# Kernel tuning notes

Hardware: AMD Instinct MI355X
Metric: run time of the kernel (lower is better)

Reference implementation:

```python
import jax, jax.numpy as jnp
import numpy as np

N_NODES = 100000
N_EDGES = 3200000
D_IN = 64
D_OUT = 64


def setup_inputs() -> dict:
    key = jax.random.key(0)
    k0, k1, k2, k3 = jax.random.split(key, 4)
    x = jax.random.normal(k0, (N_NODES, D_IN), dtype=jnp.float32)
    edge_index = jax.random.randint(k1, (2, N_EDGES), 0, N_NODES, dtype=jnp.int64)
    edge_weight = jax.random.uniform(k2, (N_EDGES,), dtype=jnp.float32)
    W = jax.random.normal(k3, (D_IN, D_OUT), dtype=jnp.float32) / jnp.sqrt(jnp.float32(D_IN))
    b = jnp.zeros((D_OUT,), dtype=jnp.float32)
    return {"x": x, "edge_index": edge_index, "edge_weight": edge_weight, "W": W, "b": b}


def reference(x, edge_index, edge_weight, W, b):
    # GiGCNConv forward: asymmetric (random-walk, D^-1 A) gcn_norm with self loops,
    # then GCNConv(normalize=False): linear -> edge-weighted scatter-add -> bias.
    N = x.shape[0]
    src, dst = edge_index[0], edge_index[1]

    # add self loops (fill value 1.0 since improved=False)
    loop = jnp.arange(N, dtype=src.dtype)
    src = jnp.concatenate([src, loop])
    dst = jnp.concatenate([dst, loop])
    ew = jnp.concatenate([edge_weight.astype(x.dtype), jnp.ones((N,), dtype=x.dtype)])

    # asymmetric normalization: in-degree (at dst) inverse scaling
    deg = jax.ops.segment_sum(ew, dst, num_segments=N)          # [N]
    deg_inv = jnp.where(deg > 0, 1.0 / deg, 0.0)                # inf -> 0
    norm = deg_inv[dst] * ew                                    # [E+N]

    # GCNConv: project then aggregate messages at destination nodes
    h = x @ W                                                   # [N, D_OUT]
    msg = norm[:, None] * h[src]                                # [E+N, D_OUT] gather
    out = jax.ops.segment_sum(msg, dst, num_segments=N)         # scatter-add
    return out + b
```

## Files before the change

### kernel.cpp

```cpp
#include <hip/hip_runtime.h>


#define D 64
#define BSH 9
#define NPB 512
#define MAXB1 256
#define BATCHA 4096
#define C1S 32
#define WSCALE 8192.0f
#define WINV (1.0f / 8192.0f)

static __device__ __forceinline__ unsigned short f2bf(float f) {
    unsigned u = __float_as_uint(f);
    u += 0x7FFFu + ((u >> 16) & 1u);
    return (unsigned short)(u >> 16);
}
static __device__ __forceinline__ float bf2f(unsigned short s) {
    return __uint_as_float(((unsigned)s) << 16);
}
static __device__ __forceinline__ float bflo(unsigned u) {
    return __uint_as_float(u << 16);
}
static __device__ __forceinline__ float bfhi(unsigned u) {
    return __uint_as_float(u & 0xFFFF0000u);
}


__global__ __launch_bounds__(256) void hist_kernel(const int* __restrict__ dst,
                                                   int* __restrict__ hist, int E, int B1) {
    __shared__ int lh[MAXB1];
    int tid = threadIdx.x;
    if (tid < MAXB1) lh[tid] = 0;
    __syncthreads();
    int t = blockIdx.x * 256 + tid;
    int stride = gridDim.x * 256;
    if ((E & 3) == 0 && (((size_t)dst & 15) == 0)) {
        const int4* d4 = (const int4*)dst;
        int n4 = E >> 2;
        for (int e = t; e < n4; e += stride) {
            int4 v = d4[e];
            atomicAdd(&lh[v.x >> BSH], 1);
            atomicAdd(&lh[v.y >> BSH], 1);
            atomicAdd(&lh[v.z >> BSH], 1);
            atomicAdd(&lh[v.w >> BSH], 1);
        }
    } else {
        for (int e = t; e < E; e += stride) {
            int d = __builtin_nontemporal_load(dst + e);
            atomicAdd(&lh[d >> BSH], 1);
        }
    }
    __syncthreads();
    if (tid < B1) {
        int v = lh[tid];
        if (v) atomicAdd(&hist[tid], v);
    }
}


__global__ __launch_bounds__(256) void scan_kernel(const int* __restrict__ hist,
                                                   int* __restrict__ off1,
                                                   int* __restrict__ cur1, int B1, int E) {
    __shared__ int s[256];
    int tid = threadIdx.x;
    int v = (tid < B1) ? hist[tid] : 0;
    s[tid] = v;
    __syncthreads();
    for (int o = 1; o < 256; o <<= 1) {
        int t = (tid >= o) ? s[tid - o] : 0;
        __syncthreads();
        s[tid] += t;
        __syncthreads();
    }
    if (tid < B1) {
        int ex = s[tid] - v;
        off1[tid] = ex;
        cur1[tid * C1S] = ex;
    }
    if (tid == 0) off1[B1] = E;
}


__global__ __launch_bounds__(256) void partA_kernel(const int* __restrict__ src,
                                                    const int* __restrict__ dst,
                                                    const float* __restrict__ ew,
                                                    int* __restrict__ cur1,
                                                    int2* __restrict__ pairs1,
                                                    int E, int nb, int aligned) {
    __shared__ int bcnt[MAXB1];
    __shared__ int bbase[MAXB1];
    __shared__ int brank[MAXB1];
    int tid = threadIdx.x;
    for (int ib = blockIdx.x; ib < nb; ib += gridDim.x) {
        int base = ib * BATCHA;
        int blen = E - base;
        if (blen > BATCHA) blen = BATCHA;
        if (tid < MAXB1) { bcnt[tid] = 0; brank[tid] = 0; }
        __syncthreads();
        int dv[16], sv[16];
        float wv[16];
        int off = tid * 16;
        if (aligned && off + 16 <= blen) {
#pragma unroll
            for (int kk = 0; kk < 4; ++kk) {
                int4 d4 = ((const int4*)(dst + base + off))[kk];
                int4 s4 = ((const int4*)(src + base + off))[kk];
                float4 w4 = ((const float4*)(ew + base + off))[kk];
                dv[kk * 4 + 0] = d4.x; dv[kk * 4 + 1] = d4.y;
                dv[kk * 4 + 2] = d4.z; dv[kk * 4 + 3] = d4.w;
                sv[kk * 4 + 0] = s4.x; sv[kk * 4 + 1] = s4.y;
                sv[kk * 4 + 2] = s4.z; sv[kk * 4 + 3] = s4.w;
                wv[kk * 4 + 0] = w4.x; wv[kk * 4 + 1] = w4.y;
                wv[kk * 4 + 2] = w4.z; wv[kk * 4 + 3] = w4.w;
            }
#pragma unroll
            for (int m = 0; m < 16; ++m) atomicAdd(&bcnt[dv[m] >> BSH], 1);
        } else {
#pragma unroll
            for (int m = 0; m < 16; ++m) {
                bool v = (off + m) < blen;
                int e = base + off + m;
                dv[m] = v ? __builtin_nontemporal_load(dst + e) : -1;
                sv[m] = v ? __builtin_nontemporal_load(src + e) : 0;
                wv[m] = v ? __builtin_nontemporal_load(ew + e) : 0.0f;
                if (v) atomicAdd(&bcnt[dv[m] >> BSH], 1);
            }
        }
        __syncthreads();
        if (tid < MAXB1 && bcnt[tid] > 0)
            bbase[tid] = atomicAdd(&cur1[tid * C1S], bcnt[tid]);
        __syncthreads();
#pragma unroll
        for (int m = 0; m < 16; ++m) {
            if (dv[m] >= 0) {
                int bin = dv[m] >> BSH;
                int r = atomicAdd(&brank[bin], 1);
                pairs1[bbase[bin] + r] =
                    make_int2(sv[m] | ((dv[m] & (NPB - 1)) << 17),
                              __float_as_int(wv[m]));
            }
        }
        __syncthreads();
    }
}


__global__ __launch_bounds__(512) void sortmerge_kernel(const int2* __restrict__ pairs1,
                                                        const int* __restrict__ off1,
                                                        unsigned* __restrict__ cw,
                                                        int* __restrict__ node_off,
                                                        int N, int B1) {
    __shared__ int lh[NPB];
    __shared__ int s[NPB];
    __shared__ int cur[NPB];
    int tid = threadIdx.x;
    int c = blockIdx.x;
    int e0 = off1[c], e1 = off1[c + 1];

    lh[tid] = 0;
    __syncthreads();

    for (int ib = e0; ib < e1; ib += 512 * 8) {
        long long pv[8];
#pragma unroll
        for (int m = 0; m < 8; ++m) {
            int i = ib + m * 512 + tid;
            pv[m] = (i < e1)
                ? __builtin_nontemporal_load((const long long*)(pairs1 + i))
                : -1LL;
        }
#pragma unroll
        for (int m = 0; m < 8; ++m) {
            int i = ib + m * 512 + tid;
            if (i < e1) atomicAdd(&lh[((int)pv[m] >> 17) & (NPB - 1)], 1);
        }
    }
    __syncthreads();

    s[tid] = lh[tid];
    __syncthreads();
    for (int o = 1; o < NPB; o <<= 1) {
        int t = (tid >= o) ? s[tid - o] : 0;
        __syncthreads();
        s[tid] += t;
        __syncthreads();
    }
    int ex = s[tid] - lh[tid];
    int gbase = c << BSH;
    if (gbase + tid <= N) node_off[gbase + tid] = e0 + ex;
    if (c == B1 - 1 && tid == 0) node_off[N] = e1;
    cur[tid] = ex;
    __syncthreads();

    for (int ib = e0; ib < e1; ib += 512 * 8) {
        long long pv[8];
#pragma unroll
        for (int m = 0; m < 8; ++m) {
            int i = ib + m * 512 + tid;
            pv[m] = (i < e1)
                ? __builtin_nontemporal_load((const long long*)(pairs1 + i))
                : -1LL;
        }
#pragma unroll
        for (int m = 0; m < 8; ++m) {
            int i = ib + m * 512 + tid;
            if (i < e1) {
                int px = (int)pv[m];
                float w = __int_as_float((int)(pv[m] >> 32));
                int node = (px >> 17) & (NPB - 1);
                int pos = atomicAdd(&cur[node], 1);
                int wq = (int)fminf(fmaxf(w, 0.0f) * WSCALE + 0.5f, 32767.0f);
                cw[e0 + pos] = (unsigned)(px & 0x1FFFF) | ((unsigned)wq << 17);
            }
        }
    }
}


__global__ __launch_bounds__(256) void gemmW_kernel(const float* __restrict__ x,
                                                    const float* __restrict__ W,
                                                    unsigned short* __restrict__ hbf, int N) {
    __shared__ float Ws[D * D];
    __shared__ float xs[32][D];
    int tid = threadIdx.x;
    int j = tid & 63;
    int g = tid >> 6;
    int base = blockIdx.x * 32;
    for (int i = tid; i < D * D; i += 256) Ws[i] = W[i];
    for (int rr = g; rr < 32; rr += 4) {
        int r = base + rr;
        if (r < N) xs[rr][j] = x[(size_t)r * D + j];
    }
    __syncthreads();
    float wc[D];
#pragma unroll
    for (int k = 0; k < D; ++k) wc[k] = Ws[k * D + j];
    for (int rr = g; rr < 32; rr += 4) {
        int r = base + rr;
        if (r < N) {
            float s0 = 0.0f, s1 = 0.0f, s2 = 0.0f, s3 = 0.0f;
#pragma unroll
            for (int k = 0; k < D; k += 4) {
                s0 = fmaf(xs[rr][k + 0], wc[k + 0], s0);
                s1 = fmaf(xs[rr][k + 1], wc[k + 1], s1);
                s2 = fmaf(xs[rr][k + 2], wc[k + 2], s2);
                s3 = fmaf(xs[rr][k + 3], wc[k + 3], s3);
            }
            hbf[(size_t)r * D + j] = f2bf((s0 + s1) + (s2 + s3));
        }
    }
}


__global__ __launch_bounds__(256) void accum_kernel(const unsigned* __restrict__ cw,
                                                    const int* __restrict__ node_off,
                                                    const unsigned short* __restrict__ hbf,
                                                    const float* __restrict__ bias,
                                                    float* __restrict__ out, int N) {
    int t = blockIdx.x * 256 + threadIdx.x;
    int n = t >> 6;
    int l = t & 63;
    if (n >= N) return;
    int eg = l >> 4;
    int cl = l & 15;
    int base = node_off[n];
    int cnt = node_off[n + 1] - base;
    const unsigned* pp = cw + base;
    const unsigned short* hcol = hbf + cl * 4;

    float a0 = 0.0f, a1 = 0.0f, a2 = 0.0f, a3 = 0.0f;
    float degs = 0.0f;
    int i = eg;
    for (; i + 12 < cnt; i += 16) {
        unsigned va = pp[i];
        unsigned vb = pp[i + 4];
        unsigned vc = pp[i + 8];
        unsigned vd = pp[i + 12];
        uint2 ha = *(const uint2*)(hcol + (size_t)(va & 0x1FFFF) * D);
        uint2 hb = *(const uint2*)(hcol + (size_t)(vb & 0x1FFFF) * D);
        uint2 hc = *(const uint2*)(hcol + (size_t)(vc & 0x1FFFF) * D);
        uint2 hd = *(const uint2*)(hcol + (size_t)(vd & 0x1FFFF) * D);
        float wa = (float)(va >> 17) * WINV;
        float wb = (float)(vb >> 17) * WINV;
        float wc = (float)(vc >> 17) * WINV;
        float wd = (float)(vd >> 17) * WINV;
        degs += (wa + wb) + (wc + wd);
        a0 = fmaf(wa, bflo(ha.x), a0);
        a1 = fmaf(wa, bfhi(ha.x), a1);
        a2 = fmaf(wa, bflo(ha.y), a2);
        a3 = fmaf(wa, bfhi(ha.y), a3);
        a0 = fmaf(wb, bflo(hb.x), a0);
        a1 = fmaf(wb, bfhi(hb.x), a1);
        a2 = fmaf(wb, bflo(hb.y), a2);
        a3 = fmaf(wb, bfhi(hb.y), a3);
        a0 = fmaf(wc, bflo(hc.x), a0);
        a1 = fmaf(wc, bfhi(hc.x), a1);
        a2 = fmaf(wc, bflo(hc.y), a2);
        a3 = fmaf(wc, bfhi(hc.y), a3);
        a0 = fmaf(wd, bflo(hd.x), a0);
        a1 = fmaf(wd, bfhi(hd.x), a1);
        a2 = fmaf(wd, bflo(hd.y), a2);
        a3 = fmaf(wd, bfhi(hd.y), a3);
    }
    for (; i < cnt; i += 4) {
        unsigned v = pp[i];
        uint2 hv = *(const uint2*)(hcol + (size_t)(v & 0x1FFFF) * D);
        float w = (float)(v >> 17) * WINV;
        degs += w;
        a0 = fmaf(w, bflo(hv.x), a0);
        a1 = fmaf(w, bfhi(hv.x), a1);
        a2 = fmaf(w, bflo(hv.y), a2);
        a3 = fmaf(w, bfhi(hv.y), a3);
    }

    a0 += __shfl_xor(a0, 16); a0 += __shfl_xor(a0, 32);
    a1 += __shfl_xor(a1, 16); a1 += __shfl_xor(a1, 32);
    a2 += __shfl_xor(a2, 16); a2 += __shfl_xor(a2, 32);
    a3 += __shfl_xor(a3, 16); a3 += __shfl_xor(a3, 32);
    degs += __shfl_xor(degs, 16); degs += __shfl_xor(degs, 32);

    if (eg == 0) {
        uint2 hs = *(const uint2*)(hcol + (size_t)n * D);
        a0 += bflo(hs.x);
        a1 += bfhi(hs.x);
        a2 += bflo(hs.y);
        a3 += bfhi(hs.y);
        degs += 1.0f;
        float di = 1.0f / degs;
        const float4 bv = *(const float4*)(bias + cl * 4);
        float4 o;
        o.x = fmaf(di, a0, bv.x);
        o.y = fmaf(di, a1, bv.y);
        o.z = fmaf(di, a2, bv.z);
        o.w = fmaf(di, a3, bv.w);
        __builtin_nontemporal_store(o.x, out + (size_t)n * D + cl * 4 + 0);
        __builtin_nontemporal_store(o.y, out + (size_t)n * D + cl * 4 + 1);
        __builtin_nontemporal_store(o.z, out + (size_t)n * D + cl * 4 + 2);
        __builtin_nontemporal_store(o.w, out + (size_t)n * D + cl * 4 + 3);
    }
}


__global__ __launch_bounds__(256) void deg_kernel(const int* __restrict__ dst,
                                                  const float* __restrict__ ew,
                                                  float* __restrict__ deg, int E) {
    int t = blockIdx.x * 256 + threadIdx.x;
    int stride = gridDim.x * 256;
    for (int e = t; e < E; e += stride) atomicAdd(&deg[dst[e]], ew[e]);
}

__global__ __launch_bounds__(256) void deginv_kernel(float* __restrict__ deg, int N) {
    int t = blockIdx.x * 256 + threadIdx.x;
    int stride = gridDim.x * 256;
    for (int n = t; n < N; n += stride) {
        float tot = deg[n] + 1.0f;
        deg[n] = (tot > 0.0f) ? (1.0f / tot) : 0.0f;
    }
}

__global__ __launch_bounds__(256) void gemm16f_kernel(const float* __restrict__ x,
                                                      const float* __restrict__ W,
                                                      float* __restrict__ h, int N) {
    __shared__ float Ws[D * D];
    __shared__ float xs[16][D];
    int tid = threadIdx.x;
    int j = tid & 63;
    int q = tid >> 6;
    int base = blockIdx.x * 16;
    for (int i = tid; i < D * D; i += 256) Ws[i] = W[i];
    for (int rr = q; rr < 16; rr += 4) {
        int r = base + rr;
        if (r < N) xs[rr][j] = x[(size_t)r * D + j];
    }
    __syncthreads();
    for (int rr = q; rr < 16; rr += 4) {
        int r = base + rr;
        if (r < N) {
            float sum = 0.0f;
#pragma unroll
            for (int k = 0; k < D; ++k) sum = fmaf(xs[rr][k], Ws[k * D + j], sum);
            h[(size_t)r * D + j] = sum;
        }
    }
}

__global__ __launch_bounds__(256) void init_kernel(const float* __restrict__ h,
                                                   const float* __restrict__ deginv,
                                                   const float* __restrict__ b,
                                                   float* __restrict__ out, int N) {
    int t = blockIdx.x * 256 + threadIdx.x;
    int stride = gridDim.x * 256;
    int nq = N * (D / 4);
    const float4* h4 = (const float4*)h;
    const float4* b4 = (const float4*)b;
    float4* o4 = (float4*)out;
    for (int q = t; q < nq; q += stride) {
        int n = q >> 4;
        int c4 = q & 15;
        float4 hv = h4[q];
        float4 bv = b4[c4];
        float di = deginv[n];
        float4 o;
        o.x = bv.x + di * hv.x;
        o.y = bv.y + di * hv.y;
        o.z = bv.z + di * hv.z;
        o.w = bv.w + di * hv.w;
        o4[q] = o;
    }
}

__global__ __launch_bounds__(256) void scatter_kernel(const int* __restrict__ src,
                                                      const int* __restrict__ dst,
                                                      const float* __restrict__ ew,
                                                      const float* __restrict__ deginv,
                                                      const float* __restrict__ h,
                                                      float* __restrict__ out, int E) {
    int t = blockIdx.x * 256 + threadIdx.x;
    int wave = t >> 6;
    int lane = t & 63;
    int nwaves = (gridDim.x * 256) >> 6;
    for (int e = wave; e < E; e += nwaves) {
        int s = src[e];
        int d = dst[e];
        float norm = deginv[d] * ew[e];
        atomicAdd(&out[d * D + lane], norm * h[s * D + lane]);
    }
}


extern "C" void kernel_launch(void* const* d_in, const int* in_sizes, int n_in,
                              void* d_out, int out_size, void* d_ws, size_t ws_size,
                              hipStream_t stream) {
    const float* x  = (const float*)d_in[0];
    const int*   ei = (const int*)d_in[1];
    const float* ew = (const float*)d_in[2];
    const float* W  = (const float*)d_in[3];
    const float* b  = (const float*)d_in[4];
    float* out = (float*)d_out;

    int N = in_sizes[0] / D;
    int E = in_sizes[2];
    const int* srcp = ei;
    const int* dstp = ei + E;

    int B1 = (N + NPB - 1) >> BSH;

    size_t ints_n = 256 + 320 + (size_t)MAXB1 * C1S + ((size_t)N + 64);
    size_t p1_off  = ((ints_n * 4) + 255) & ~(size_t)255;
    size_t hbf_off = (p1_off + (size_t)E * 8 + 255) & ~(size_t)255;
    size_t cw_off  = (hbf_off + (size_t)N * D * 2 + 255) & ~(size_t)255;
    size_t need = cw_off + (size_t)E * 4;

    if (N <= 131072 && ws_size >= need) {
        int* hist     = (int*)d_ws;
        int* off1     = hist + 256;
        int* cur1     = off1 + 320;
        int* node_off = cur1 + (size_t)MAXB1 * C1S;
        int2* pairs1  = (int2*)((char*)d_ws + p1_off);
        unsigned short* hbf = (unsigned short*)((char*)d_ws + hbf_off);
        unsigned* cw  = (unsigned*)((char*)d_ws + cw_off);

        int aligned = (((E & 3) == 0) && (((size_t)dstp & 15) == 0)) ? 1 : 0;

        hipMemsetAsync(hist, 0, 256 * 4, stream);
        hist_kernel<<<1024, 256, 0, stream>>>(dstp, hist, E, B1);
        scan_kernel<<<1, 256, 0, stream>>>(hist, off1, cur1, B1, E);
        int nb = (E + BATCHA - 1) / BATCHA;
        int gA = nb < 2048 ? nb : 2048;
        partA_kernel<<<gA, 256, 0, stream>>>(srcp, dstp, ew, cur1, pairs1, E, nb, aligned);
        sortmerge_kernel<<<B1, 512, 0, stream>>>(pairs1, off1, cw, node_off, N, B1);
        gemmW_kernel<<<(N + 31) / 32, 256, 0, stream>>>(x, W, hbf, N);
        accum_kernel<<<(N + 3) / 4, 256, 0, stream>>>(cw, node_off, hbf, b, out, N);
    } else {
        size_t Npad = ((size_t)N + 63) & ~(size_t)63;
        float* deg = (float*)d_ws;
        float* h = deg + Npad;
        hipMemsetAsync(deg, 0, (size_t)N * sizeof(float), stream);
        deg_kernel<<<2048, 256, 0, stream>>>(dstp, ew, deg, E);
        deginv_kernel<<<(N + 255) / 256, 256, 0, stream>>>(deg, N);
        gemm16f_kernel<<<(N + 15) / 16, 256, 0, stream>>>(x, W, h, N);
        init_kernel<<<2048, 256, 0, stream>>>(h, deg, b, out, N);
        scatter_kernel<<<2048, 256, 0, stream>>>(srcp, dstp, ew, deg, h, out, E);
    }
}
```

Baseline: 192.6 us.

## Split bucketed edge pairs into packed cw words plus 16-bit local dst

partA now packs source index and quantized weight into a 32-bit word and writes the node-local destination as a separate 16-bit array, replacing the 8-byte int2 pairs. sortmerge reads only the 2-byte array for its histogram pass and moves the packed word directly in the scatter pass, with no requantization. The aim is to cut intermediate memory traffic between the partition and sort stages. Partition batches also double to 32 edges per thread and the histogram grid is halved, which raises register pressure and lowers parallelism per launch.

```diff
diff --git a/kernel.cpp b/kernel.cpp
--- a/kernel.cpp
+++ b/kernel.cpp
@@ -5,7 +5,7 @@
 #define BSH 9
 #define NPB 512
 #define MAXB1 256
-#define BATCHA 4096
+#define BATCHA 8192
 #define C1S 32
 #define WSCALE 8192.0f
 #define WINV (1.0f / 8192.0f)
@@ -15,14 +15,15 @@
     u += 0x7FFFu + ((u >> 16) & 1u);
     return (unsigned short)(u >> 16);
 }
-static __device__ __forceinline__ float bf2f(unsigned short s) {
-    return __uint_as_float(((unsigned)s) << 16);
-}
 static __device__ __forceinline__ float bflo(unsigned u) {
     return __uint_as_float(u << 16);
 }
 static __device__ __forceinline__ float bfhi(unsigned u) {
     return __uint_as_float(u & 0xFFFF0000u);
+}
+static __device__ __forceinline__ unsigned packcw(int s, float w) {
+    int wq = (int)fminf(fmaxf(w, 0.0f) * WSCALE + 0.5f, 32767.0f);
+    return (unsigned)s | ((unsigned)wq << 17);
 }
 
 
@@ -85,7 +86,8 @@
                                                     const int* __restrict__ dst,
                                                     const float* __restrict__ ew,
                                                     int* __restrict__ cur1,
-                                                    int2* __restrict__ pairs1,
+                                                    unsigned* __restrict__ cw0,
+                                                    unsigned short* __restrict__ dls,
                                                     int E, int nb, int aligned) {
     __shared__ int bcnt[MAXB1];
     __shared__ int bbase[MAXB1];
@@ -97,33 +99,41 @@
         if (blen > BATCHA) blen = BATCHA;
         if (tid < MAXB1) { bcnt[tid] = 0; brank[tid] = 0; }
         __syncthreads();
-        int dv[16], sv[16];
-        float wv[16];
-        int off = tid * 16;
-        if (aligned && off + 16 <= blen) {
-#pragma unroll
-            for (int kk = 0; kk < 4; ++kk) {
+        unsigned cwq[32];
+        int meta[32];
+        int off = tid * 32;
+        if (aligned && off + 32 <= blen) {
+#pragma unroll
+            for (int kk = 0; kk < 8; ++kk) {
                 int4 d4 = ((const int4*)(dst + base + off))[kk];
                 int4 s4 = ((const int4*)(src + base + off))[kk];
                 float4 w4 = ((const float4*)(ew + base + off))[kk];
-                dv[kk * 4 + 0] = d4.x; dv[kk * 4 + 1] = d4.y;
-                dv[kk * 4 + 2] = d4.z; dv[kk * 4 + 3] = d4.w;
-                sv[kk * 4 + 0] = s4.x; sv[kk * 4 + 1] = s4.y;
-                sv[kk * 4 + 2] = s4.z; sv[kk * 4 + 3] = s4.w;
-                wv[kk * 4 + 0] = w4.x; wv[kk * 4 + 1] = w4.y;
-                wv[kk * 4 + 2] = w4.z; wv[kk * 4 + 3] = w4.w;
-            }
-#pragma unroll
-            for (int m = 0; m < 16; ++m) atomicAdd(&bcnt[dv[m] >> BSH], 1);
+                cwq[kk * 4 + 0] = packcw(s4.x, w4.x);
+                cwq[kk * 4 + 1] = packcw(s4.y, w4.y);
+                cwq[kk * 4 + 2] = packcw(s4.z, w4.z);
+                cwq[kk * 4 + 3] = packcw(s4.w, w4.w);
+                meta[kk * 4 + 0] = d4.x;
+                meta[kk * 4 + 1] = d4.y;
+                meta[kk * 4 + 2] = d4.z;
+                meta[kk * 4 + 3] = d4.w;
+            }
+#pragma unroll
+            for (int m = 0; m < 32; ++m) atomicAdd(&bcnt[meta[m] >> BSH], 1);
         } else {
 #pragma unroll
-            for (int m = 0; m < 16; ++m) {
+            for (int m = 0; m < 32; ++m) {
                 bool v = (off + m) < blen;
                 int e = base + off + m;
-                dv[m] = v ? __builtin_nontemporal_load(dst + e) : -1;
-                sv[m] = v ? __builtin_nontemporal_load(src + e) : 0;
-                wv[m] = v ? __builtin_nontemporal_load(ew + e) : 0.0f;
-                if (v) atomicAdd(&bcnt[dv[m] >> BSH], 1);
+                if (v) {
+                    int d = __builtin_nontemporal_load(dst + e);
+                    int s = __builtin_nontemporal_load(src + e);
+                    float w = __builtin_nontemporal_load(ew + e);
+                    cwq[m] = packcw(s, w);
+                    meta[m] = d;
+                    atomicAdd(&bcnt[d >> BSH], 1);
+                } else {
+                    meta[m] = -1;
+                }
             }
         }
         __syncthreads();
@@ -131,21 +141,22 @@
             bbase[tid] = atomicAdd(&cur1[tid * C1S], bcnt[tid]);
         __syncthreads();
 #pragma unroll
-        for (int m = 0; m < 16; ++m) {
-            if (dv[m] >= 0) {
-                int bin = dv[m] >> BSH;
+        for (int m = 0; m < 32; ++m) {
+            if (meta[m] >= 0) {
+                int bin = meta[m] >> BSH;
                 int r = atomicAdd(&brank[bin], 1);
-                pairs1[bbase[bin] + r] =
-                    make_int2(sv[m] | ((dv[m] & (NPB - 1)) << 17),
-                              __float_as_int(wv[m]));
-            }
-        }
-        __syncthreads();
-    }
-}
-
-
-__global__ __launch_bounds__(512) void sortmerge_kernel(const int2* __restrict__ pairs1,
+                int pos = bbase[bin] + r;
+                cw0[pos] = cwq[m];
+                dls[pos] = (unsigned short)(meta[m] & (NPB - 1));
+            }
+        }
+        __syncthreads();
+    }
+}
+
+
+__global__ __launch_bounds__(512) void sortmerge_kernel(const unsigned* __restrict__ cw0,
+                                                        const unsigned short* __restrict__ dls,
                                                         const int* __restrict__ off1,
                                                         unsigned* __restrict__ cw,
                                                         int* __restrict__ node_off,
@@ -161,19 +172,15 @@
     __syncthreads();
 
     for (int ib = e0; ib < e1; ib += 512 * 8) {
-        long long pv[8];
+        int dlv[8];
 #pragma unroll
         for (int m = 0; m < 8; ++m) {
             int i = ib + m * 512 + tid;
-            pv[m] = (i < e1)
-                ? __builtin_nontemporal_load((const long long*)(pairs1 + i))
-                : -1LL;
-        }
-#pragma unroll
-        for (int m = 0; m < 8; ++m) {
-            int i = ib + m * 512 + tid;
-            if (i < e1) atomicAdd(&lh[((int)pv[m] >> 17) & (NPB - 1)], 1);
-        }
+            dlv[m] = (i < e1) ? (int)__builtin_nontemporal_load(dls + i) : -1;
+        }
+#pragma unroll
+        for (int m = 0; m < 8; ++m)
+            if (dlv[m] >= 0) atomicAdd(&lh[dlv[m]], 1);
     }
     __syncthreads();
 
@@ -193,24 +200,23 @@
     __syncthreads();
 
     for (int ib = e0; ib < e1; ib += 512 * 8) {
-        long long pv[8];
-#pragma unroll
-        for (int m = 0; m < 8; ++m) {
-            int i = ib + m * 512 + tid;
-            pv[m] = (i < e1)
-                ? __builtin_nontemporal_load((const long long*)(pairs1 + i))
-                : -1LL;
-        }
+        unsigned cv[8];
+        int dlv[8];
 #pragma unroll
         for (int m = 0; m < 8; ++m) {
             int i = ib + m * 512 + tid;
             if (i < e1) {
-                int px = (int)pv[m];
-                float w = __int_as_float((int)(pv[m] >> 32));
-                int node = (px >> 17) & (NPB - 1);
-                int pos = atomicAdd(&cur[node], 1);
-                int wq = (int)fminf(fmaxf(w, 0.0f) * WSCALE + 0.5f, 32767.0f);
-                cw[e0 + pos] = (unsigned)(px & 0x1FFFF) | ((unsigned)wq << 17);
+                cv[m] = __builtin_nontemporal_load(cw0 + i);
+                dlv[m] = (int)__builtin_nontemporal_load(dls + i);
+            } else {
+                dlv[m] = -1;
+            }
+        }
+#pragma unroll
+        for (int m = 0; m < 8; ++m) {
+            if (dlv[m] >= 0) {
+                int pos = atomicAdd(&cur[dlv[m]], 1);
+                cw[e0 + pos] = cv[m];
             }
         }
     }
@@ -446,8 +452,9 @@
     int B1 = (N + NPB - 1) >> BSH;
 
     size_t ints_n = 256 + 320 + (size_t)MAXB1 * C1S + ((size_t)N + 64);
-    size_t p1_off  = ((ints_n * 4) + 255) & ~(size_t)255;
-    size_t hbf_off = (p1_off + (size_t)E * 8 + 255) & ~(size_t)255;
+    size_t cw0_off = ((ints_n * 4) + 255) & ~(size_t)255;
+    size_t dls_off = (cw0_off + (size_t)E * 4 + 255) & ~(size_t)255;
+    size_t hbf_off = (dls_off + (size_t)E * 2 + 255) & ~(size_t)255;
     size_t cw_off  = (hbf_off + (size_t)N * D * 2 + 255) & ~(size_t)255;
     size_t need = cw_off + (size_t)E * 4;
 
@@ -456,19 +463,20 @@
         int* off1     = hist + 256;
         int* cur1     = off1 + 320;
         int* node_off = cur1 + (size_t)MAXB1 * C1S;
-        int2* pairs1  = (int2*)((char*)d_ws + p1_off);
+        unsigned* cw0 = (unsigned*)((char*)d_ws + cw0_off);
+        unsigned short* dls = (unsigned short*)((char*)d_ws + dls_off);
         unsigned short* hbf = (unsigned short*)((char*)d_ws + hbf_off);
         unsigned* cw  = (unsigned*)((char*)d_ws + cw_off);
 
         int aligned = (((E & 3) == 0) && (((size_t)dstp & 15) == 0)) ? 1 : 0;
 
         hipMemsetAsync(hist, 0, 256 * 4, stream);
-        hist_kernel<<<1024, 256, 0, stream>>>(dstp, hist, E, B1);
+        hist_kernel<<<512, 256, 0, stream>>>(dstp, hist, E, B1);
         scan_kernel<<<1, 256, 0, stream>>>(hist, off1, cur1, B1, E);
         int nb = (E + BATCHA - 1) / BATCHA;
         int gA = nb < 2048 ? nb : 2048;
-        partA_kernel<<<gA, 256, 0, stream>>>(srcp, dstp, ew, cur1, pairs1, E, nb, aligned);
-        sortmerge_kernel<<<B1, 512, 0, stream>>>(pairs1, off1, cw, node_off, N, B1);
+        partA_kernel<<<gA, 256, 0, stream>>>(srcp, dstp, ew, cur1, cw0, dls, E, nb, aligned);
+        sortmerge_kernel<<<B1, 512, 0, stream>>>(cw0, dls, off1, cw, node_off, N, B1);
         gemmW_kernel<<<(N + 31) / 32, 256, 0, stream>>>(x, W, hbf, N);
         accum_kernel<<<(N + 3) / 4, 256, 0, stream>>>(cw, node_off, hbf, b, out, N);
     } else {
```

After: 198.8 us. 3.2% more time.
